# Performance work log

Hardware: AMD Instinct MI355X
Metric: run time of the kernel (lower is better)

The kernel has to match this reference:

```python
import jax, jax.numpy as jnp
import numpy as np

N_NODES = 200000
N_EDGES = 600000
F_IN, F_HID, F_OUT = 165, 128, 2


def gcn_conv(x, edge_index, W, b):
    # PyG GCNConv: add self-loops, symmetric deg^{-1/2} normalization,
    # linear transform, scatter-add aggregation (src -> dst), then bias.
    N = x.shape[0]
    loop = jnp.arange(N, dtype=edge_index.dtype)
    src = jnp.concatenate([edge_index[0], loop])
    dst = jnp.concatenate([edge_index[1], loop])
    deg = jax.ops.segment_sum(jnp.ones_like(dst, dtype=x.dtype), dst, num_segments=N)
    dinv = jnp.where(deg > 0, jax.lax.rsqrt(jnp.maximum(deg, 1e-12)), 0.0)
    norm = dinv[src] * dinv[dst]              # [E+N]
    h = x @ W                                  # [N, out]
    msg = h[src] * norm[:, None]               # gather + scale
    out = jax.ops.segment_sum(msg, dst, num_segments=N)  # scatter-add
    return out + b


def setup_inputs() -> dict:
    key = jax.random.key(0)
    k1, k2, k3, k4, k5 = jax.random.split(key, 5)
    x = jax.random.normal(k1, (N_NODES, F_IN), dtype=jnp.float32)
    edge_index = jax.random.randint(k2, (2, N_EDGES), 0, N_NODES, dtype=jnp.int64)
    # Glorot-style init for GCN weights, zero bias (as in PyG GCNConv).
    W1 = jax.random.normal(k3, (F_IN, F_HID), dtype=jnp.float32) / np.sqrt(F_IN)
    b1 = jnp.zeros((F_HID,), dtype=jnp.float32)
    W2 = jax.random.normal(k4, (F_HID, F_OUT), dtype=jnp.float32) / np.sqrt(F_HID)
    b2 = jnp.zeros((F_OUT,), dtype=jnp.float32)
    return {"x": x, "edge_index": edge_index, "W1": W1, "b1": b1, "W2": W2, "b2": b2}


def reference(x, edge_index, W1, b1, W2, b2):
    h = gcn_conv(x, edge_index, W1, b1)
    h = jax.nn.relu(h)
    # dropout(p=0.5) is identity in eval mode
    out = gcn_conv(h, edge_index, W2, b2)
    return out
```

## Files before the change

kernel.cpp:

```cpp
#include <hip/hip_runtime.h>

#define N_NODES 200000
#define N_EDGES 600000
#define F_IN 165
#define F_HID 128
#define KP 200
#define NT 6250

typedef short short8 __attribute__((ext_vector_type(8)));
typedef float f32x4 __attribute__((ext_vector_type(4)));

__device__ __forceinline__ unsigned short f2bf(float f) {
  union { float f; unsigned int u; } v; v.f = f;
  unsigned int u = v.u;
  return (unsigned short)((u + 0x7FFFu + ((u >> 16) & 1u)) >> 16);
}
__device__ __forceinline__ float bflo(unsigned int v) {
  union { unsigned int u; float f; } x; x.u = v << 16; return x.f;
}
__device__ __forceinline__ float bfhi(unsigned int v) {
  union { unsigned int u; float f; } x; x.u = v & 0xffff0000u; return x.f;
}

__global__ void k_zero(int* __restrict__ cnt) {
  int i = blockIdx.x * 256 + threadIdx.x;
  if (i < N_NODES) cnt[i] = 0;
}

__global__ void k_count(const int* __restrict__ ei, int* __restrict__ cnt) {
  int e = blockIdx.x * 256 + threadIdx.x;
  if (e < N_EDGES) atomicAdd(&cnt[ei[N_EDGES + e]], 1);
}

__global__ void k_scan1(const int* __restrict__ cnt, int* __restrict__ rowptr, int* __restrict__ bsum) {
  __shared__ int sd[256];
  int t = threadIdx.x;
  int idx = blockIdx.x * 256 + t;
  int v = (idx < N_NODES) ? cnt[idx] : 0;
  sd[t] = v; __syncthreads();
  #pragma unroll
  for (int off = 1; off < 256; off <<= 1) {
    int u = (t >= off) ? sd[t - off] : 0;
    __syncthreads();
    sd[t] += u;
    __syncthreads();
  }
  if (idx < N_NODES) rowptr[idx] = sd[t] - v;
  if (t == 255) bsum[blockIdx.x] = sd[t];
}

__global__ void k_scan2(int* __restrict__ bsum, int nb) {
  __shared__ int sd[1024];
  int t = threadIdx.x;
  int v = (t < nb) ? bsum[t] : 0;
  sd[t] = v; __syncthreads();
  for (int off = 1; off < 1024; off <<= 1) {
    int u = (t >= off) ? sd[t - off] : 0;
    __syncthreads();
    sd[t] += u;
    __syncthreads();
  }
  if (t < nb) bsum[t] = sd[t] - v;
}

__global__ void k_scan3(const int* __restrict__ cnt, const int* __restrict__ bsum,
                        int* __restrict__ rowptr, int* __restrict__ fill, float* __restrict__ dinv) {
  int idx = blockIdx.x * 256 + threadIdx.x;
  if (idx < N_NODES) {
    int rp = rowptr[idx] + bsum[blockIdx.x];
    rowptr[idx] = rp;
    fill[idx] = rp;
    dinv[idx] = rsqrtf((float)(cnt[idx] + 1));
  }
  if (idx == 0) rowptr[N_NODES] = N_EDGES;
}

__global__ void k_fill(const int* __restrict__ ei, int* __restrict__ fill, int* __restrict__ srcl) {
  int e = blockIdx.x * 256 + threadIdx.x;
  if (e < N_EDGES) {
    int d = ei[N_EDGES + e];
    int s = ei[e];
    int slot = atomicAdd(&fill[d], 1);
    srcl[slot] = s;
  }
}

__global__ void k_wt(const float* __restrict__ W1, unsigned short* __restrict__ wt) {
  int idx = blockIdx.x * 256 + threadIdx.x;
  if (idx < F_HID * KP) {
    int c = idx / KP, k = idx - c * KP;
    wt[idx] = (k < F_IN) ? f2bf(W1[k * F_HID + c]) : (unsigned short)0;
  }
}

__global__ __launch_bounds__(256) void k_gemm1(const float* __restrict__ x,
                                               const unsigned short* __restrict__ wt,
                                               const float* __restrict__ dinv,
                                               unsigned short* __restrict__ h16) {
  __shared__ unsigned short Bs[F_HID * KP];
  __shared__ unsigned short As[32 * KP];
  int tid = threadIdx.x;

  const uint4* wt4 = (const uint4*)wt;
  uint4* Bs4 = (uint4*)Bs;
  #pragma unroll 4
  for (int j = tid; j < F_HID * KP / 8; j += 256) Bs4[j] = wt4[j];

  for (int j = tid; j < 32 * (KP - F_IN); j += 256) {
    int r = j / (KP - F_IN), c = F_IN + (j - (j / (KP - F_IN)) * (KP - F_IN));
    As[r * KP + c] = 0;
  }

  int t = blockIdx.x;
  int G = gridDim.x;

  {
    const float4* x4 = (const float4*)(x + (long)t * 32 * F_IN);
    for (int j = tid; j < 32 * F_IN / 4; j += 256) {
      float4 v = x4[j];
      int e = 4 * j;
      #pragma unroll
      for (int u = 0; u < 4; ++u) {
        int ee = e + u;
        int r = ee / F_IN, c = ee - r * F_IN;
        As[r * KP + c] = f2bf((&v.x)[u]);
      }
    }
  }
  __syncthreads();

  int lane = tid & 63;
  int w = tid >> 6;
  int rg = w & 1;
  int ch = w >> 1;
  int arow = rg * 16 + (lane & 15);
  int kg = (lane >> 4) * 8;

  while (t < NT) {
    int tn = t + G;
    bool have = tn < NT;

    float4 vals[6];
    if (have) {
      const float4* x4 = (const float4*)(x + (long)tn * 32 * F_IN);
      #pragma unroll
      for (int i = 0; i < 6; ++i) {
        int j = tid + i * 256;
        if (j < 32 * F_IN / 4) vals[i] = x4[j];
      }
    }

    f32x4 acc[4];
    #pragma unroll
    for (int i = 0; i < 4; ++i) acc[i] = (f32x4){0.f, 0.f, 0.f, 0.f};
    #pragma unroll
    for (int ks = 0; ks < 6; ++ks) {
      short8 af = *(const short8*)(&As[arow * KP + ks * 32 + kg]);
      #pragma unroll
      for (int cb = 0; cb < 4; ++cb) {
        int col = (ch * 4 + cb) * 16 + (lane & 15);
        short8 bf = *(const short8*)(&Bs[col * KP + ks * 32 + kg]);
        acc[cb] = __builtin_amdgcn_mfma_f32_16x16x32_bf16(af, bf, acc[cb], 0, 0, 0);
      }
    }
    long orow = (long)t * 32 + rg * 16 + (lane >> 4) * 4;
    int ocol = lane & 15;
    float dv[4];
    #pragma unroll
    for (int j = 0; j < 4; ++j) dv[j] = dinv[orow + j];
    #pragma unroll
    for (int cb = 0; cb < 4; ++cb) {
      #pragma unroll
      for (int j = 0; j < 4; ++j) {
        h16[(orow + j) * F_HID + (ch * 4 + cb) * 16 + ocol] = f2bf(acc[cb][j] * dv[j]);
      }
    }
    __syncthreads();

    if (have) {
      #pragma unroll
      for (int i = 0; i < 6; ++i) {
        int j = tid + i * 256;
        if (j < 32 * F_IN / 4) {
          int e = 4 * j;
          #pragma unroll
          for (int u = 0; u < 4; ++u) {
            int ee = e + u;
            int r = ee / F_IN, c = ee - r * F_IN;
            As[r * KP + c] = f2bf((&vals[i].x)[u]);
          }
        }
      }
    }
    __syncthreads();
    t = tn;
  }
}

__global__ __launch_bounds__(256) void k_agg1(const unsigned int* __restrict__ H,
                                              const float* __restrict__ dinv,
                                              const int* __restrict__ rowptr, const int* __restrict__ srcl,
                                              const float* __restrict__ b1, const float* __restrict__ W2,
                                              float* __restrict__ h2s) {
  int tid = threadIdx.x;
  int local = tid >> 6;
  int lane = tid & 63;
  int d = blockIdx.x * 4 + local;

  unsigned int v = H[(long)d * 64 + lane];
  float acc0 = bflo(v), acc1 = bfhi(v);
  int r0 = rowptr[d], r1 = rowptr[d + 1];
  int n = r1 - r0;
  for (int b = 0; b < n; b += 4) {
    int i0 = r0 + b;
    bool m1 = b + 1 < n, m2 = b + 2 < n, m3 = b + 3 < n;
    int s0 = srcl[i0];
    int s1 = m1 ? srcl[i0 + 1] : s0;
    int s2 = m2 ? srcl[i0 + 2] : s0;
    int s3 = m3 ? srcl[i0 + 3] : s0;
    unsigned int v0 = H[(long)s0 * 64 + lane];
    unsigned int v1 = H[(long)s1 * 64 + lane];
    unsigned int v2 = H[(long)s2 * 64 + lane];
    unsigned int v3 = H[(long)s3 * 64 + lane];
    acc0 += bflo(v0);                      acc1 += bfhi(v0);
    acc0 = fmaf(m1 ? 1.f : 0.f, bflo(v1), acc0); acc1 = fmaf(m1 ? 1.f : 0.f, bfhi(v1), acc1);
    acc0 = fmaf(m2 ? 1.f : 0.f, bflo(v2), acc0); acc1 = fmaf(m2 ? 1.f : 0.f, bfhi(v2), acc1);
    acc0 = fmaf(m3 ? 1.f : 0.f, bflo(v3), acc0); acc1 = fmaf(m3 ? 1.f : 0.f, bfhi(v3), acc1);
  }
  float dd = dinv[d];
  float2 bb = ((const float2*)b1)[lane];
  float a0 = fmaxf(fmaf(acc0, dd, bb.x), 0.f);
  float a1 = fmaxf(fmaf(acc1, dd, bb.y), 0.f);
  float4 w2 = ((const float4*)W2)[lane];
  float p0 = a0 * w2.x + a1 * w2.z;
  float p1 = a0 * w2.y + a1 * w2.w;
  #pragma unroll
  for (int off = 32; off > 0; off >>= 1) {
    p0 += __shfl_down(p0, off);
    p1 += __shfl_down(p1, off);
  }
  if (lane == 0) ((float2*)h2s)[d] = make_float2(p0 * dd, p1 * dd);
}

__global__ void k_agg2(const float* __restrict__ h2s, const float* __restrict__ dinv,
                       const int* __restrict__ rowptr, const int* __restrict__ srcl,
                       const float* __restrict__ b2, float* __restrict__ out) {
  int d = blockIdx.x * 256 + threadIdx.x;
  if (d >= N_NODES) return;
  const float2* G = (const float2*)h2s;
  float2 g = G[d];
  float o0 = g.x, o1 = g.y;
  int r0 = rowptr[d], r1 = rowptr[d + 1];
  int n = r1 - r0;
  for (int b = 0; b < n; b += 4) {
    int i0 = r0 + b;
    bool m1 = b + 1 < n, m2 = b + 2 < n, m3 = b + 3 < n;
    int s0 = srcl[i0];
    int s1 = m1 ? srcl[i0 + 1] : s0;
    int s2 = m2 ? srcl[i0 + 2] : s0;
    int s3 = m3 ? srcl[i0 + 3] : s0;
    float2 g0 = G[s0], g1 = G[s1], g2 = G[s2], g3 = G[s3];
    o0 += g0.x;                   o1 += g0.y;
    o0 = fmaf(m1 ? 1.f : 0.f, g1.x, o0); o1 = fmaf(m1 ? 1.f : 0.f, g1.y, o1);
    o0 = fmaf(m2 ? 1.f : 0.f, g2.x, o0); o1 = fmaf(m2 ? 1.f : 0.f, g2.y, o1);
    o0 = fmaf(m3 ? 1.f : 0.f, g3.x, o0); o1 = fmaf(m3 ? 1.f : 0.f, g3.y, o1);
  }
  float dd = dinv[d];
  ((float2*)out)[d] = make_float2(fmaf(o0, dd, b2[0]), fmaf(o1, dd, b2[1]));
}

extern "C" void kernel_launch(void* const* d_in, const int* in_sizes, int n_in,
                              void* d_out, int out_size, void* d_ws, size_t ws_size,
                              hipStream_t stream) {
  const float* x  = (const float*)d_in[0];
  const int*   ei = (const int*)d_in[1];
  const float* W1 = (const float*)d_in[2];
  const float* b1 = (const float*)d_in[3];
  const float* W2 = (const float*)d_in[4];
  const float* b2 = (const float*)d_in[5];
  float* out = (float*)d_out;

  char* p = (char*)d_ws;
  size_t off = 0;
  auto take = [&](size_t bytes) -> void* {
    void* r = p + off;
    off += (bytes + 255) & ~(size_t)255;
    return r;
  };
  unsigned short* h16    = (unsigned short*)take((size_t)N_NODES * F_HID * 2);
  unsigned short* wt     = (unsigned short*)take((size_t)F_HID * KP * 2);
  float*          h2s    = (float*)take((size_t)N_NODES * 2 * 4);
  int*            cnt    = (int*)take((size_t)N_NODES * 4);
  int*            fill   = (int*)take((size_t)N_NODES * 4);
  int*            rowptr = (int*)take(((size_t)N_NODES + 1) * 4);
  int*            srcl   = (int*)take(((size_t)N_EDGES + 8) * 4);
  float*          dinv   = (float*)take((size_t)N_NODES * 4);
  int*            bsum   = (int*)take(4096);
  (void)ws_size; (void)in_sizes; (void)n_in; (void)out_size;

  int nbE = (N_EDGES + 255) / 256;
  int nbN = (N_NODES + 255) / 256;
  k_zero<<<nbN, 256, 0, stream>>>(cnt);
  k_count<<<nbE, 256, 0, stream>>>(ei, cnt);
  k_scan1<<<nbN, 256, 0, stream>>>(cnt, rowptr, bsum);
  k_scan2<<<1, 1024, 0, stream>>>(bsum, nbN);
  k_scan3<<<nbN, 256, 0, stream>>>(cnt, bsum, rowptr, fill, dinv);
  k_fill<<<nbE, 256, 0, stream>>>(ei, fill, srcl);
  k_wt<<<(F_HID * KP + 255) / 256, 256, 0, stream>>>(W1, wt);
  k_gemm1<<<512, 256, 0, stream>>>(x, wt, dinv, h16);
  k_agg1<<<N_NODES / 4, 256, 0, stream>>>((const unsigned int*)h16, dinv, rowptr, srcl, b1, W2, h2s);
  k_agg2<<<nbN, 256, 0, stream>>>(h2s, dinv, rowptr, srcl, b2, out);
}
```

Measured before the change: 185.0 us.

## Keep W1 fragments in registers, swap MFMA operands for packed stores, raise grid

The bf16 weight tile is no longer staged in shared memory. Each wave now loads its 4x6 MFMA weight fragments into registers once, which cuts the 51 KB LDS footprint so more blocks fit per CU (launch bounds 2, grid 768). The MFMA operands are swapped so each lane owns one row and four consecutive columns, which allows packed 8-byte bf16 stores and a single dinv load per lane instead of scattered 2-byte stores. The cost is 24 extra VGPR quads per thread, which raises register pressure.

```diff
diff --git a/kernel.cpp b/kernel.cpp
--- a/kernel.cpp
+++ b/kernel.cpp
@@ -93,18 +93,29 @@
   }
 }
 
-__global__ __launch_bounds__(256) void k_gemm1(const float* __restrict__ x,
-                                               const unsigned short* __restrict__ wt,
-                                               const float* __restrict__ dinv,
-                                               unsigned short* __restrict__ h16) {
-  __shared__ unsigned short Bs[F_HID * KP];
+__global__ __launch_bounds__(256, 2) void k_gemm1(const float* __restrict__ x,
+                                                  const unsigned short* __restrict__ wt,
+                                                  const float* __restrict__ dinv,
+                                                  unsigned short* __restrict__ h16) {
   __shared__ unsigned short As[32 * KP];
   int tid = threadIdx.x;
-
-  const uint4* wt4 = (const uint4*)wt;
-  uint4* Bs4 = (uint4*)Bs;
-  #pragma unroll 4
-  for (int j = tid; j < F_HID * KP / 8; j += 256) Bs4[j] = wt4[j];
+  int lane = tid & 63;
+  int w = tid >> 6;
+  int rg = w & 1;
+  int cw = w >> 1;
+
+  short8 wf[4][6];
+  {
+    int c0 = cw * 64 + (lane & 15);
+    int kq = (lane >> 4) * 8;
+    #pragma unroll
+    for (int cb = 0; cb < 4; ++cb) {
+      #pragma unroll
+      for (int ks = 0; ks < 6; ++ks) {
+        wf[cb][ks] = *(const short8*)(&wt[(c0 + cb * 16) * KP + ks * 32 + kq]);
+      }
+    }
+  }
 
   for (int j = tid; j < 32 * (KP - F_IN); j += 256) {
     int r = j / (KP - F_IN), c = F_IN + (j - (j / (KP - F_IN)) * (KP - F_IN));
@@ -129,12 +140,8 @@
   }
   __syncthreads();
 
-  int lane = tid & 63;
-  int w = tid >> 6;
-  int rg = w & 1;
-  int ch = w >> 1;
   int arow = rg * 16 + (lane & 15);
-  int kg = (lane >> 4) * 8;
+  int kq = (lane >> 4) * 8;
 
   while (t < NT) {
     int tn = t + G;
@@ -155,25 +162,21 @@
     for (int i = 0; i < 4; ++i) acc[i] = (f32x4){0.f, 0.f, 0.f, 0.f};
     #pragma unroll
     for (int ks = 0; ks < 6; ++ks) {
-      short8 af = *(const short8*)(&As[arow * KP + ks * 32 + kg]);
+      short8 xf = *(const short8*)(&As[arow * KP + ks * 32 + kq]);
       #pragma unroll
       for (int cb = 0; cb < 4; ++cb) {
-        int col = (ch * 4 + cb) * 16 + (lane & 15);
-        short8 bf = *(const short8*)(&Bs[col * KP + ks * 32 + kg]);
-        acc[cb] = __builtin_amdgcn_mfma_f32_16x16x32_bf16(af, bf, acc[cb], 0, 0, 0);
-      }
-    }
-    long orow = (long)t * 32 + rg * 16 + (lane >> 4) * 4;
-    int ocol = lane & 15;
-    float dv[4];
-    #pragma unroll
-    for (int j = 0; j < 4; ++j) dv[j] = dinv[orow + j];
+        acc[cb] = __builtin_amdgcn_mfma_f32_16x16x32_bf16(wf[cb][ks], xf, acc[cb], 0, 0, 0);
+      }
+    }
+    long row = (long)t * 32 + arow;
+    float dd = dinv[row];
+    unsigned short* hp = &h16[row * F_HID + cw * 64 + (lane >> 4) * 4];
     #pragma unroll
     for (int cb = 0; cb < 4; ++cb) {
-      #pragma unroll
-      for (int j = 0; j < 4; ++j) {
-        h16[(orow + j) * F_HID + (ch * 4 + cb) * 16 + ocol] = f2bf(acc[cb][j] * dv[j]);
-      }
+      unsigned int p0 = (unsigned int)f2bf(acc[cb][0] * dd) | ((unsigned int)f2bf(acc[cb][1] * dd) << 16);
+      unsigned int p1 = (unsigned int)f2bf(acc[cb][2] * dd) | ((unsigned int)f2bf(acc[cb][3] * dd) << 16);
+      uint2 pp; pp.x = p0; pp.y = p1;
+      *(uint2*)(hp + cb * 16) = pp;
     }
     __syncthreads();
 
@@ -307,7 +310,7 @@
   k_scan3<<<nbN, 256, 0, stream>>>(cnt, bsum, rowptr, fill, dinv);
   k_fill<<<nbE, 256, 0, stream>>>(ei, fill, srcl);
   k_wt<<<(F_HID * KP + 255) / 256, 256, 0, stream>>>(W1, wt);
-  k_gemm1<<<512, 256, 0, stream>>>(x, wt, dinv, h16);
+  k_gemm1<<<768, 256, 0, stream>>>(x, wt, dinv, h16);
   k_agg1<<<N_NODES / 4, 256, 0, stream>>>((const unsigned int*)h16, dinv, rowptr, srcl, b1, W2, h2s);
   k_agg2<<<nbN, 256, 0, stream>>>(h2s, dinv, rowptr, srcl, b2, out);
 }
```

New measurement: 189.8 us. +2.6%, slower.

## Fuse CSR build, GEMM and aggregations into two cooperative grid-synced kernels

Applied to the files above, without the earlier changes.

Replaces ten separate kernel launches with two cooperative kernels that use grid-wide barriers between phases: one covers counting, scanning, CSR fill, weight transpose and the bf16 GEMM, the other covers both aggregation layers. The scan is restructured so each thread handles two nodes, which lets 512 blocks cover all nodes and a single block scan the block sums. The goal is to remove launch gaps and the tail idle time between many small kernels. In exchange, fixed grid sizes limit parallelism in the atomic and aggregation phases, grid.sync adds barrier cost, and the 64KB LDS kernel must fit co-resident for a cooperative launch to succeed.

```diff
diff --git a/kernel.cpp b/kernel.cpp
--- a/kernel.cpp
+++ b/kernel.cpp
@@ -1,4 +1,7 @@
 #include <hip/hip_runtime.h>
+#include <hip/hip_cooperative_groups.h>
+
+namespace cg = cooperative_groups;
 
 #define N_NODES 200000
 #define N_EDGES 600000
@@ -6,6 +9,9 @@
 #define F_HID 128
 #define KP 200
 #define NT 6250
+#define G1 512
+#define GT1 (G1 * 256)
+#define G2 1024
 
 typedef short short8 __attribute__((ext_vector_type(8)));
 typedef float f32x4 __attribute__((ext_vector_type(4)));
@@ -22,98 +28,99 @@
   union { unsigned int u; float f; } x; x.u = v & 0xffff0000u; return x.f;
 }
 
-__global__ void k_zero(int* __restrict__ cnt) {
-  int i = blockIdx.x * 256 + threadIdx.x;
-  if (i < N_NODES) cnt[i] = 0;
-}
-
-__global__ void k_count(const int* __restrict__ ei, int* __restrict__ cnt) {
-  int e = blockIdx.x * 256 + threadIdx.x;
-  if (e < N_EDGES) atomicAdd(&cnt[ei[N_EDGES + e]], 1);
-}
-
-__global__ void k_scan1(const int* __restrict__ cnt, int* __restrict__ rowptr, int* __restrict__ bsum) {
-  __shared__ int sd[256];
-  int t = threadIdx.x;
-  int idx = blockIdx.x * 256 + t;
-  int v = (idx < N_NODES) ? cnt[idx] : 0;
-  sd[t] = v; __syncthreads();
+__global__ __launch_bounds__(256) void k_fused1(const float* __restrict__ x,
+                                                const int* __restrict__ ei,
+                                                const float* __restrict__ W1,
+                                                int* __restrict__ cnt,
+                                                int* __restrict__ bsum,
+                                                int* __restrict__ rowptr,
+                                                int* __restrict__ fill,
+                                                int* __restrict__ srcl,
+                                                float* __restrict__ dinv,
+                                                unsigned short* __restrict__ wt,
+                                                unsigned short* __restrict__ h16) {
+  cg::grid_group grid = cg::this_grid();
+  __shared__ unsigned short Bs[F_HID * KP];
+  __shared__ unsigned short As[32 * KP];
+  int tid = threadIdx.x, bid = blockIdx.x;
+  int g = bid * 256 + tid;
+
+  for (int i = g; i < N_NODES; i += GT1) cnt[i] = 0;
+  for (int i = g; i < F_HID * KP; i += GT1) {
+    int c = i / KP, k = i - c * KP;
+    wt[i] = (k < F_IN) ? f2bf(W1[k * F_HID + c]) : (unsigned short)0;
+  }
+  grid.sync();
+
+  for (int e = g; e < N_EDGES; e += GT1) atomicAdd(&cnt[ei[N_EDGES + e]], 1);
+  {
+    const uint4* wt4 = (const uint4*)wt;
+    uint4* Bs4 = (uint4*)Bs;
+    for (int j = tid; j < F_HID * KP / 8; j += 256) Bs4[j] = wt4[j];
+  }
+  grid.sync();
+
+  int i0 = 2 * g;
+  int c0 = (i0 < N_NODES) ? cnt[i0] : 0;
+  int c1 = (i0 + 1 < N_NODES) ? cnt[i0 + 1] : 0;
+  int mysum = c0 + c1;
+  int* sd = (int*)As;
+  sd[tid] = mysum;
+  __syncthreads();
   #pragma unroll
   for (int off = 1; off < 256; off <<= 1) {
-    int u = (t >= off) ? sd[t - off] : 0;
-    __syncthreads();
-    sd[t] += u;
-    __syncthreads();
-  }
-  if (idx < N_NODES) rowptr[idx] = sd[t] - v;
-  if (t == 255) bsum[blockIdx.x] = sd[t];
-}
-
-__global__ void k_scan2(int* __restrict__ bsum, int nb) {
-  __shared__ int sd[1024];
-  int t = threadIdx.x;
-  int v = (t < nb) ? bsum[t] : 0;
-  sd[t] = v; __syncthreads();
-  for (int off = 1; off < 1024; off <<= 1) {
-    int u = (t >= off) ? sd[t - off] : 0;
-    __syncthreads();
-    sd[t] += u;
-    __syncthreads();
-  }
-  if (t < nb) bsum[t] = sd[t] - v;
-}
-
-__global__ void k_scan3(const int* __restrict__ cnt, const int* __restrict__ bsum,
-                        int* __restrict__ rowptr, int* __restrict__ fill, float* __restrict__ dinv) {
-  int idx = blockIdx.x * 256 + threadIdx.x;
-  if (idx < N_NODES) {
-    int rp = rowptr[idx] + bsum[blockIdx.x];
-    rowptr[idx] = rp;
-    fill[idx] = rp;
-    dinv[idx] = rsqrtf((float)(cnt[idx] + 1));
-  }
-  if (idx == 0) rowptr[N_NODES] = N_EDGES;
-}
-
-__global__ void k_fill(const int* __restrict__ ei, int* __restrict__ fill, int* __restrict__ srcl) {
-  int e = blockIdx.x * 256 + threadIdx.x;
-  if (e < N_EDGES) {
+    int u = (tid >= off) ? sd[tid - off] : 0;
+    __syncthreads();
+    sd[tid] += u;
+    __syncthreads();
+  }
+  int myoff = sd[tid] - mysum;
+  if (tid == 255) bsum[bid] = sd[tid];
+  grid.sync();
+
+  if (bid == 0) {
+    int a = bsum[2 * tid], b = bsum[2 * tid + 1];
+    int ps = a + b;
+    __syncthreads();
+    sd[tid] = ps;
+    __syncthreads();
+    #pragma unroll
+    for (int off = 1; off < 256; off <<= 1) {
+      int u = (tid >= off) ? sd[tid - off] : 0;
+      __syncthreads();
+      sd[tid] += u;
+      __syncthreads();
+    }
+    int ex = sd[tid] - ps;
+    bsum[2 * tid] = ex;
+    bsum[2 * tid + 1] = ex + a;
+  }
+  grid.sync();
+
+  int base = bsum[bid] + myoff;
+  if (i0 < N_NODES) {
+    rowptr[i0] = base; fill[i0] = base;
+    dinv[i0] = rsqrtf((float)(c0 + 1));
+  }
+  if (i0 + 1 < N_NODES) {
+    int b2 = base + c0;
+    rowptr[i0 + 1] = b2; fill[i0 + 1] = b2;
+    dinv[i0 + 1] = rsqrtf((float)(c1 + 1));
+  }
+  if (g == 0) rowptr[N_NODES] = N_EDGES;
+  grid.sync();
+
+  for (int e = g; e < N_EDGES; e += GT1) {
     int d = ei[N_EDGES + e];
     int s = ei[e];
-    int slot = atomicAdd(&fill[d], 1);
-    srcl[slot] = s;
-  }
-}
-
-__global__ void k_wt(const float* __restrict__ W1, unsigned short* __restrict__ wt) {
-  int idx = blockIdx.x * 256 + threadIdx.x;
-  if (idx < F_HID * KP) {
-    int c = idx / KP, k = idx - c * KP;
-    wt[idx] = (k < F_IN) ? f2bf(W1[k * F_HID + c]) : (unsigned short)0;
-  }
-}
-
-__global__ __launch_bounds__(256) void k_gemm1(const float* __restrict__ x,
-                                               const unsigned short* __restrict__ wt,
-                                               const float* __restrict__ dinv,
-                                               unsigned short* __restrict__ h16) {
-  __shared__ unsigned short Bs[F_HID * KP];
-  __shared__ unsigned short As[32 * KP];
-  int tid = threadIdx.x;
-
-  const uint4* wt4 = (const uint4*)wt;
-  uint4* Bs4 = (uint4*)Bs;
-  #pragma unroll 4
-  for (int j = tid; j < F_HID * KP / 8; j += 256) Bs4[j] = wt4[j];
+    srcl[atomicAdd(&fill[d], 1)] = s;
+  }
 
   for (int j = tid; j < 32 * (KP - F_IN); j += 256) {
     int r = j / (KP - F_IN), c = F_IN + (j - (j / (KP - F_IN)) * (KP - F_IN));
     As[r * KP + c] = 0;
   }
-
-  int t = blockIdx.x;
-  int G = gridDim.x;
-
+  int t = bid;
   {
     const float4* x4 = (const float4*)(x + (long)t * 32 * F_IN);
     for (int j = tid; j < 32 * F_IN / 4; j += 256) {
@@ -137,7 +144,7 @@
   int kg = (lane >> 4) * 8;
 
   while (t < NT) {
-    int tn = t + G;
+    int tn = t + G1;
     bool have = tn < NT;
 
     float4 vals[6];
@@ -197,76 +204,80 @@
   }
 }
 
-__global__ __launch_bounds__(256) void k_agg1(const unsigned int* __restrict__ H,
-                                              const float* __restrict__ dinv,
-                                              const int* __restrict__ rowptr, const int* __restrict__ srcl,
-                                              const float* __restrict__ b1, const float* __restrict__ W2,
-                                              float* __restrict__ h2s) {
+__global__ __launch_bounds__(256, 4) void k_fused2(const unsigned int* __restrict__ H,
+                                                   const float* __restrict__ dinv,
+                                                   const int* __restrict__ rowptr,
+                                                   const int* __restrict__ srcl,
+                                                   const float* __restrict__ b1,
+                                                   const float* __restrict__ W2,
+                                                   const float* __restrict__ b2,
+                                                   float* __restrict__ h2s,
+                                                   float* __restrict__ out) {
+  cg::grid_group grid = cg::this_grid();
   int tid = threadIdx.x;
   int local = tid >> 6;
   int lane = tid & 63;
-  int d = blockIdx.x * 4 + local;
-
-  unsigned int v = H[(long)d * 64 + lane];
-  float acc0 = bflo(v), acc1 = bfhi(v);
-  int r0 = rowptr[d], r1 = rowptr[d + 1];
-  int n = r1 - r0;
-  for (int b = 0; b < n; b += 4) {
-    int i0 = r0 + b;
-    bool m1 = b + 1 < n, m2 = b + 2 < n, m3 = b + 3 < n;
-    int s0 = srcl[i0];
-    int s1 = m1 ? srcl[i0 + 1] : s0;
-    int s2 = m2 ? srcl[i0 + 2] : s0;
-    int s3 = m3 ? srcl[i0 + 3] : s0;
-    unsigned int v0 = H[(long)s0 * 64 + lane];
-    unsigned int v1 = H[(long)s1 * 64 + lane];
-    unsigned int v2 = H[(long)s2 * 64 + lane];
-    unsigned int v3 = H[(long)s3 * 64 + lane];
-    acc0 += bflo(v0);                      acc1 += bfhi(v0);
-    acc0 = fmaf(m1 ? 1.f : 0.f, bflo(v1), acc0); acc1 = fmaf(m1 ? 1.f : 0.f, bfhi(v1), acc1);
-    acc0 = fmaf(m2 ? 1.f : 0.f, bflo(v2), acc0); acc1 = fmaf(m2 ? 1.f : 0.f, bfhi(v2), acc1);
-    acc0 = fmaf(m3 ? 1.f : 0.f, bflo(v3), acc0); acc1 = fmaf(m3 ? 1.f : 0.f, bfhi(v3), acc1);
-  }
-  float dd = dinv[d];
-  float2 bb = ((const float2*)b1)[lane];
-  float a0 = fmaxf(fmaf(acc0, dd, bb.x), 0.f);
-  float a1 = fmaxf(fmaf(acc1, dd, bb.y), 0.f);
-  float4 w2 = ((const float4*)W2)[lane];
-  float p0 = a0 * w2.x + a1 * w2.z;
-  float p1 = a0 * w2.y + a1 * w2.w;
-  #pragma unroll
-  for (int off = 32; off > 0; off >>= 1) {
-    p0 += __shfl_down(p0, off);
-    p1 += __shfl_down(p1, off);
-  }
-  if (lane == 0) ((float2*)h2s)[d] = make_float2(p0 * dd, p1 * dd);
-}
-
-__global__ void k_agg2(const float* __restrict__ h2s, const float* __restrict__ dinv,
-                       const int* __restrict__ rowptr, const int* __restrict__ srcl,
-                       const float* __restrict__ b2, float* __restrict__ out) {
-  int d = blockIdx.x * 256 + threadIdx.x;
-  if (d >= N_NODES) return;
-  const float2* G = (const float2*)h2s;
-  float2 g = G[d];
-  float o0 = g.x, o1 = g.y;
-  int r0 = rowptr[d], r1 = rowptr[d + 1];
-  int n = r1 - r0;
-  for (int b = 0; b < n; b += 4) {
-    int i0 = r0 + b;
-    bool m1 = b + 1 < n, m2 = b + 2 < n, m3 = b + 3 < n;
-    int s0 = srcl[i0];
-    int s1 = m1 ? srcl[i0 + 1] : s0;
-    int s2 = m2 ? srcl[i0 + 2] : s0;
-    int s3 = m3 ? srcl[i0 + 3] : s0;
-    float2 g0 = G[s0], g1 = G[s1], g2 = G[s2], g3 = G[s3];
-    o0 += g0.x;                   o1 += g0.y;
-    o0 = fmaf(m1 ? 1.f : 0.f, g1.x, o0); o1 = fmaf(m1 ? 1.f : 0.f, g1.y, o1);
-    o0 = fmaf(m2 ? 1.f : 0.f, g2.x, o0); o1 = fmaf(m2 ? 1.f : 0.f, g2.y, o1);
-    o0 = fmaf(m3 ? 1.f : 0.f, g3.x, o0); o1 = fmaf(m3 ? 1.f : 0.f, g3.y, o1);
-  }
-  float dd = dinv[d];
-  ((float2*)out)[d] = make_float2(fmaf(o0, dd, b2[0]), fmaf(o1, dd, b2[1]));
+
+  for (int d4 = blockIdx.x; d4 < N_NODES / 4; d4 += G2) {
+    int d = d4 * 4 + local;
+    unsigned int v = H[(long)d * 64 + lane];
+    float acc0 = bflo(v), acc1 = bfhi(v);
+    int r0 = rowptr[d], r1 = rowptr[d + 1];
+    int n = r1 - r0;
+    for (int b = 0; b < n; b += 4) {
+      int i0 = r0 + b;
+      bool m1 = b + 1 < n, m2 = b + 2 < n, m3 = b + 3 < n;
+      int s0 = srcl[i0];
+      int s1 = m1 ? srcl[i0 + 1] : s0;
+      int s2 = m2 ? srcl[i0 + 2] : s0;
+      int s3 = m3 ? srcl[i0 + 3] : s0;
+      unsigned int v0 = H[(long)s0 * 64 + lane];
+      unsigned int v1 = H[(long)s1 * 64 + lane];
+      unsigned int v2 = H[(long)s2 * 64 + lane];
+      unsigned int v3 = H[(long)s3 * 64 + lane];
+      acc0 += bflo(v0);                            acc1 += bfhi(v0);
+      acc0 = fmaf(m1 ? 1.f : 0.f, bflo(v1), acc0); acc1 = fmaf(m1 ? 1.f : 0.f, bfhi(v1), acc1);
+      acc0 = fmaf(m2 ? 1.f : 0.f, bflo(v2), acc0); acc1 = fmaf(m2 ? 1.f : 0.f, bfhi(v2), acc1);
+      acc0 = fmaf(m3 ? 1.f : 0.f, bflo(v3), acc0); acc1 = fmaf(m3 ? 1.f : 0.f, bfhi(v3), acc1);
+    }
+    float dd = dinv[d];
+    float2 bb = ((const float2*)b1)[lane];
+    float a0 = fmaxf(fmaf(acc0, dd, bb.x), 0.f);
+    float a1 = fmaxf(fmaf(acc1, dd, bb.y), 0.f);
+    float4 w2 = ((const float4*)W2)[lane];
+    float p0 = a0 * w2.x + a1 * w2.z;
+    float p1 = a0 * w2.y + a1 * w2.w;
+    #pragma unroll
+    for (int off = 32; off > 0; off >>= 1) {
+      p0 += __shfl_down(p0, off);
+      p1 += __shfl_down(p1, off);
+    }
+    if (lane == 0) ((float2*)h2s)[d] = make_float2(p0 * dd, p1 * dd);
+  }
+  grid.sync();
+
+  const float2* Gv = (const float2*)h2s;
+  for (int d = blockIdx.x * 256 + tid; d < N_NODES; d += G2 * 256) {
+    float2 gv = Gv[d];
+    float o0 = gv.x, o1 = gv.y;
+    int r0 = rowptr[d], r1 = rowptr[d + 1];
+    int n = r1 - r0;
+    for (int b = 0; b < n; b += 4) {
+      int i0 = r0 + b;
+      bool m1 = b + 1 < n, m2 = b + 2 < n, m3 = b + 3 < n;
+      int s0 = srcl[i0];
+      int s1 = m1 ? srcl[i0 + 1] : s0;
+      int s2 = m2 ? srcl[i0 + 2] : s0;
+      int s3 = m3 ? srcl[i0 + 3] : s0;
+      float2 g0 = Gv[s0], g1 = Gv[s1], g2 = Gv[s2], g3 = Gv[s3];
+      o0 += g0.x;                          o1 += g0.y;
+      o0 = fmaf(m1 ? 1.f : 0.f, g1.x, o0); o1 = fmaf(m1 ? 1.f : 0.f, g1.y, o1);
+      o0 = fmaf(m2 ? 1.f : 0.f, g2.x, o0); o1 = fmaf(m2 ? 1.f : 0.f, g2.y, o1);
+      o0 = fmaf(m3 ? 1.f : 0.f, g3.x, o0); o1 = fmaf(m3 ? 1.f : 0.f, g3.y, o1);
+    }
+    float dd = dinv[d];
+    ((float2*)out)[d] = make_float2(fmaf(o0, dd, b2[0]), fmaf(o1, dd, b2[1]));
+  }
 }
 
 extern "C" void kernel_launch(void* const* d_in, const int* in_sizes, int n_in,
@@ -295,19 +306,17 @@
   int*            rowptr = (int*)take(((size_t)N_NODES + 1) * 4);
   int*            srcl   = (int*)take(((size_t)N_EDGES + 8) * 4);
   float*          dinv   = (float*)take((size_t)N_NODES * 4);
-  int*            bsum   = (int*)take(4096);
+  int*            bsum   = (int*)take((size_t)G1 * 4);
   (void)ws_size; (void)in_sizes; (void)n_in; (void)out_size;
 
-  int nbE = (N_EDGES + 255) / 256;
-  int nbN = (N_NODES + 255) / 256;
-  k_zero<<<nbN, 256, 0, stream>>>(cnt);
-  k_count<<<nbE, 256, 0, stream>>>(ei, cnt);
-  k_scan1<<<nbN, 256, 0, stream>>>(cnt, rowptr, bsum);
-  k_scan2<<<1, 1024, 0, stream>>>(bsum, nbN);
-  k_scan3<<<nbN, 256, 0, stream>>>(cnt, bsum, rowptr, fill, dinv);
-  k_fill<<<nbE, 256, 0, stream>>>(ei, fill, srcl);
-  k_wt<<<(F_HID * KP + 255) / 256, 256, 0, stream>>>(W1, wt);
-  k_gemm1<<<512, 256, 0, stream>>>(x, wt, dinv, h16);
-  k_agg1<<<N_NODES / 4, 256, 0, stream>>>((const unsigned int*)h16, dinv, rowptr, srcl, b1, W2, h2s);
-  k_agg2<<<nbN, 256, 0, stream>>>(h2s, dinv, rowptr, srcl, b2, out);
-}
+  const unsigned int* H = (const unsigned int*)h16;
+
+  void* a1[] = {(void*)&x, (void*)&ei, (void*)&W1, (void*)&cnt, (void*)&bsum,
+                (void*)&rowptr, (void*)&fill, (void*)&srcl, (void*)&dinv,
+                (void*)&wt, (void*)&h16};
+  hipLaunchCooperativeKernel((const void*)k_fused1, dim3(G1), dim3(256), a1, 0, stream);
+
+  void* a2[] = {(void*)&H, (void*)&dinv, (void*)&rowptr, (void*)&srcl,
+                (void*)&b1, (void*)&W2, (void*)&b2, (void*)&h2s, (void*)&out};
+  hipLaunchCooperativeKernel((const void*)k_fused2, dim3(G2), dim3(256), a2, 0, stream);
+}
```

After: 600.5 us. 225% more time.
